# Kernel tuning notes

Measured on AMD Instinct MI355X. Metric: run time of the kernel, lower is better.

Reference implementation:

```python
import jax, jax.numpy as jnp
import numpy as np

N = 50000
E = 800000
DIN = 64
DOUT = 64
H = 4
C = DOUT // H
EPS = 1e-5


def setup_inputs() -> dict:
    key = jax.random.key(0)
    ks = jax.random.split(key, 40)
    inp = {}
    inp["x"] = jax.random.normal(ks[0], (N, DIN), jnp.float32)
    inp["edge_index"] = jax.random.randint(ks[1], (2, E), 0, N, dtype=jnp.int32)
    inp["edge_weight"] = jax.random.uniform(ks[2], (E,), jnp.float32)
    inp["edge_attr"] = jax.random.normal(ks[3], (E, 1), jnp.float32)
    k = 4
    for i in range(2):
        din = DIN if i == 0 else DOUT
        s = din ** -0.5
        inp[f"gcn_w{i}"] = jax.random.normal(ks[k], (din, DOUT), jnp.float32) * s; k += 1
        inp[f"gcn_b{i}"] = jnp.zeros((DOUT,), jnp.float32)
        inp[f"res_w{i}"] = jax.random.normal(ks[k], (din, DOUT), jnp.float32) * s; k += 1
        inp[f"res_b{i}"] = jnp.zeros((DOUT,), jnp.float32)
        inp[f"ln_g{i}"] = jnp.ones((DOUT,), jnp.float32)
        inp[f"ln_b{i}"] = jnp.zeros((DOUT,), jnp.float32)
        sg = DOUT ** -0.5
        inp[f"gat_w{i}"] = jax.random.normal(ks[k], (DOUT, H * C), jnp.float32) * sg; k += 1
        inp[f"gat_b{i}"] = jnp.zeros((H * C,), jnp.float32)
        inp[f"att_src{i}"] = jax.random.normal(ks[k], (H, C), jnp.float32) * (C ** -0.5); k += 1
        inp[f"att_dst{i}"] = jax.random.normal(ks[k], (H, C), jnp.float32) * (C ** -0.5); k += 1
        inp[f"att_e{i}"] = jax.random.normal(ks[k], (H, C), jnp.float32) * (C ** -0.5); k += 1
        inp[f"ew_w{i}"] = jax.random.normal(ks[k], (1, H * C), jnp.float32); k += 1
    return inp


def _gcn(x, src0, dst0, ew, W, b):
    n = x.shape[0]
    sl = jnp.arange(n, dtype=src0.dtype)
    src = jnp.concatenate([src0, sl])
    dst = jnp.concatenate([dst0, sl])
    w = jnp.concatenate([ew, jnp.ones((n,), ew.dtype)])  # self-loop weight 1
    deg = jax.ops.segment_sum(w, dst, num_segments=n)
    dinv = jnp.where(deg > 0, jax.lax.rsqrt(deg), 0.0)
    norm = dinv[src] * w * dinv[dst]
    h = x @ W  # [n, DOUT]
    out = jax.ops.segment_sum(h[src] * norm[:, None], dst, num_segments=n)
    return out + b


def _gat(x, src0, dst0, ea, W, b, a_src, a_dst, a_e, We):
    n = x.shape[0]
    sl = jnp.arange(n, dtype=src0.dtype)
    src = jnp.concatenate([src0, sl])
    dst = jnp.concatenate([dst0, sl])
    loop_attr = jnp.broadcast_to(ea.mean(axis=0, keepdims=True), (n, ea.shape[1]))
    ea2 = jnp.concatenate([ea, loop_attr], axis=0)  # fill_value='mean'
    xl = (x @ W).reshape(n, H, C)
    a_s = (xl * a_src).sum(-1)  # [n,H]
    a_d = (xl * a_dst).sum(-1)
    a_ee = ((ea2 @ We).reshape(-1, H, C) * a_e).sum(-1)  # [E2,H]
    alpha = jax.nn.leaky_relu(a_s[src] + a_d[dst] + a_ee, 0.2)
    m = jax.ops.segment_max(alpha, dst, num_segments=n)
    e = jnp.exp(alpha - m[dst])
    s = jax.ops.segment_sum(e, dst, num_segments=n)
    alpha = e / (s[dst] + 1e-16)
    out = jax.ops.segment_sum(xl[src] * alpha[:, :, None], dst, num_segments=n)
    return out.reshape(n, H * C) + b


def _ln(x, g, b):
    mu = x.mean(-1, keepdims=True)
    v = ((x - mu) ** 2).mean(-1, keepdims=True)
    return (x - mu) * jax.lax.rsqrt(v + EPS) * g + b


def reference(x, edge_index, edge_weight, edge_attr,
              gcn_w0, gcn_b0, res_w0, res_b0, ln_g0, ln_b0,
              gat_w0, gat_b0, att_src0, att_dst0, att_e0, ew_w0,
              gcn_w1, gcn_b1, res_w1, res_b1, ln_g1, ln_b1,
              gat_w1, gat_b1, att_src1, att_dst1, att_e1, ew_w1):
    src0, dst0 = edge_index[0], edge_index[1]
    layers = [
        (gcn_w0, gcn_b0, res_w0, res_b0, ln_g0, ln_b0, gat_w0, gat_b0, att_src0, att_dst0, att_e0, ew_w0),
        (gcn_w1, gcn_b1, res_w1, res_b1, ln_g1, ln_b1, gat_w1, gat_b1, att_src1, att_dst1, att_e1, ew_w1),
    ]
    for (gw, gb, rw, rb, lg, lb, Wg, bg, a_s, a_d, a_e, We) in layers:
        residual = x @ rw + rb
        x = jax.nn.silu(_gcn(x, src0, dst0, edge_weight, gw, gb)) + residual
        x = _ln(x, lg, lb)
        x = jax.nn.silu(_gat(x, src0, dst0, edge_attr, Wg, bg, a_s, a_d, a_e, We)) + x
    return x  # down_sample=False -> Identity
```

## Files before the change

### kernel.cpp

```cpp
#include <hip/hip_runtime.h>
#include <hip/hip_fp16.h>

#define NN 50000
#define NE 800000
#define D 64
#define EPS 1e-5f
#define NT 3125
#define NB1 250
#define EPB 3200
#define NBIN 196
#define STOT 49152
#define SBLK 192

typedef unsigned short ushort_t;
typedef unsigned int uint_t;
typedef __attribute__((ext_vector_type(8))) short bf16x8;
typedef __attribute__((ext_vector_type(4))) float f32x4;

__device__ __forceinline__ float wave_sum64(float v) {
#pragma unroll
  for (int m = 1; m <= 32; m <<= 1) v += __shfl_xor(v, m, 64);
  return v;
}
__device__ __forceinline__ int wave_sum64i(int v) {
#pragma unroll
  for (int m = 1; m <= 32; m <<= 1) v += __shfl_xor(v, m, 64);
  return v;
}
__device__ __forceinline__ float group_sum16(float v) {
#pragma unroll
  for (int m = 1; m <= 8; m <<= 1) v += __shfl_xor(v, m, 64);
  return v;
}
__device__ __forceinline__ float silu_f(float v) { return v / (1.f + __expf(-v)); }
__device__ __forceinline__ float lrelu_f(float v) { return v >= 0.f ? v : 0.2f * v; }
__device__ __forceinline__ ushort_t f2b(float x) {
  unsigned u = __float_as_uint(x);
  return (ushort_t)((u + 0x7FFFu + ((u >> 16) & 1u)) >> 16);
}
__device__ __forceinline__ float b2f(ushort_t u) {
  return __uint_as_float(((unsigned)u) << 16);
}
__device__ __forceinline__ ushort_t f2h(float x) {
  return __half_as_ushort(__float2half_rn(x));
}
__device__ __forceinline__ float h2f(unsigned u) {
  return __half2float(__ushort_as_half((ushort_t)(u & 0xFFFFu)));
}
__device__ __forceinline__ float sel4(float a, float b, float c, float d, int h) {
  float ab = (h & 1) ? b : a;
  float cd = (h & 1) ? d : c;
  return (h & 2) ? cd : ab;
}
__device__ __forceinline__ bf16x8 pack8(float4 a, float4 b) {
  bf16x8 r;
  r[0] = (short)f2b(a.x); r[1] = (short)f2b(a.y);
  r[2] = (short)f2b(a.z); r[3] = (short)f2b(a.w);
  r[4] = (short)f2b(b.x); r[5] = (short)f2b(b.y);
  r[6] = (short)f2b(b.z); r[7] = (short)f2b(b.w);
  return r;
}

__global__ void __launch_bounds__(256) k_pre(
    const int* __restrict__ ei, int* __restrict__ histG,
    const float* __restrict__ x, const float* __restrict__ W1,
    const float* __restrict__ W2, const float* __restrict__ b2,
    ushort_t* __restrict__ out1, float* __restrict__ out2) {
  __shared__ __align__(16) char smem[16384];
  if (blockIdx.x < NB1) {
    int* h = (int*)smem;
    int blk = blockIdx.x;
    for (int j = threadIdx.x; j < NBIN; j += 256) h[j] = 0;
    __syncthreads();
    int e0 = blk * EPB;
    for (int e = e0 + threadIdx.x; e < e0 + EPB; e += 256)
      atomicAdd(&h[ei[NE + e] >> 8], 1);
    __syncthreads();
    for (int j = threadIdx.x; j < NBIN; j += 256) histG[j * NB1 + blk] = h[j];
    return;
  }
  ushort_t* wf = (ushort_t*)smem;
  for (int e = threadIdx.x; e < 8192; e += 256) {
    int f = e >> 9, r = e & 511;
    int lane = r >> 3, j = r & 7;
    int m = f >> 3, s = (f >> 2) & 1, t = f & 3;
    int k = s * 32 + (lane >> 4) * 8 + j;
    int n = t * 16 + (lane & 15);
    const float* Wm = m ? W2 : W1;
    wf[e] = f2b(Wm[k * D + n]);
  }
  __syncthreads();
  int tile = (blockIdx.x - NB1) * 4 + (threadIdx.x >> 6);
  if (tile >= NT) return;
  int l = threadIdx.x & 63;
  int q = l >> 4, cn = l & 15;
  const float* xr = x + ((size_t)tile * 16 + cn) * D + q * 8;
  float4 xa = *(const float4*)xr;
  float4 xb = *(const float4*)(xr + 4);
  float4 xc = *(const float4*)(xr + 32);
  float4 xd = *(const float4*)(xr + 36);
  bf16x8 a0 = pack8(xa, xb), a1 = pack8(xc, xd);
  f32x4 acc1[4], acc2[4];
#pragma unroll
  for (int t = 0; t < 4; ++t) {
    bf16x8 b10 = *(const bf16x8*)&wf[(0 * 8 + 0 * 4 + t) * 512 + l * 8];
    bf16x8 b11 = *(const bf16x8*)&wf[(0 * 8 + 1 * 4 + t) * 512 + l * 8];
    bf16x8 b20 = *(const bf16x8*)&wf[(1 * 8 + 0 * 4 + t) * 512 + l * 8];
    bf16x8 b21 = *(const bf16x8*)&wf[(1 * 8 + 1 * 4 + t) * 512 + l * 8];
    f32x4 z = {0.f, 0.f, 0.f, 0.f};
    acc1[t] = __builtin_amdgcn_mfma_f32_16x16x32_bf16(a0, b10, z, 0, 0, 0);
    acc1[t] = __builtin_amdgcn_mfma_f32_16x16x32_bf16(a1, b11, acc1[t], 0, 0, 0);
    acc2[t] = __builtin_amdgcn_mfma_f32_16x16x32_bf16(a0, b20, z, 0, 0, 0);
    acc2[t] = __builtin_amdgcn_mfma_f32_16x16x32_bf16(a1, b21, acc2[t], 0, 0, 0);
  }
#pragma unroll
  for (int t = 0; t < 4; ++t) {
    float bb = b2[t * 16 + cn];
#pragma unroll
    for (int r = 0; r < 4; ++r) {
      size_t row = (size_t)tile * 16 + q * 4 + r;
      out1[row * D + t * 16 + cn] = f2b(acc1[t][r]);
      out2[row * D + t * 16 + cn] = acc2[t][r] + bb;
    }
  }
}

__global__ void __launch_bounds__(256) k_scanA(
    int* __restrict__ histG, int* __restrict__ bsum, float* __restrict__ scal,
    const float* __restrict__ Wg0, const float* __restrict__ Wg1,
    const float* __restrict__ W11, const float* __restrict__ W21,
    const float* __restrict__ We0, const float* __restrict__ ae0,
    const float* __restrict__ We1, const float* __restrict__ ae1,
    ushort_t* __restrict__ wg16, ushort_t* __restrict__ wd16,
    float* __restrict__ wea2) {
  if (blockIdx.x == SBLK) {
    int tid = threadIdx.x;
    for (int t = tid; t < 1024; t += 256) scal[t] = 0.f;
    for (int e = tid; e < 4096; e += 256) {
      int f = e >> 9, r = e & 511;
      int lane = r >> 3, j = r & 7;
      int s = (f >> 2) & 1, t = f & 3;
      int k = s * 32 + (lane >> 4) * 8 + j;
      int n = t * 16 + (lane & 15);
      wg16[e] = f2b(Wg0[k * D + n]);
      wg16[4096 + e] = f2b(Wg1[k * D + n]);
    }
    for (int e = tid; e < 8192; e += 256) {
      int f = e >> 9, r = e & 511;
      int lane = r >> 3, j = r & 7;
      int m = f >> 3, s = (f >> 2) & 1, t = f & 3;
      int k = s * 32 + (lane >> 4) * 8 + j;
      int n = t * 16 + (lane & 15);
      const float* Wm = m ? W21 : W11;
      wd16[e] = f2b(Wm[k * D + n]);
    }
    if (tid < 64) {
      float v = group_sum16(We0[tid] * ae0[tid]);
      if ((tid & 15) == 0) wea2[tid >> 4] = v;
    } else if (tid < 128) {
      int c = tid - 64;
      float v = group_sum16(We1[c] * ae1[c]);
      if ((c & 15) == 0) wea2[4 + (c >> 4)] = v;
    }
    return;
  }
  __shared__ int sm[256];
  int j = threadIdx.x;
  int i = blockIdx.x * 256 + j;
  const int TOT = NBIN * NB1;
  int v = (i < TOT) ? histG[i] : 0;
  sm[j] = v;
  __syncthreads();
  for (int off = 1; off < 256; off <<= 1) {
    int t = (j >= off) ? sm[j - off] : 0;
    __syncthreads();
    sm[j] += t;
    __syncthreads();
  }
  if (i < TOT) histG[i] = sm[j] - v;
  if (j == 255) bsum[blockIdx.x] = sm[255];
}

__global__ void __launch_bounds__(256) k_scanC(int* __restrict__ histG,
                                               const int* __restrict__ bsum) {
  __shared__ int ws4[4];
  int t = threadIdx.x;
  int v = (t < (int)blockIdx.x) ? bsum[t] : 0;
  v = wave_sum64i(v);
  if ((t & 63) == 0) ws4[t >> 6] = v;
  __syncthreads();
  int prefix = ws4[0] + ws4[1] + ws4[2] + ws4[3];
  int i = blockIdx.x * 256 + t;
  if (i < NBIN * NB1) histG[i] += prefix;
}

__global__ void __launch_bounds__(256) k_part(
    const int* __restrict__ ei, const float* __restrict__ ew,
    const float* __restrict__ ea, const int* __restrict__ histG,
    uint2* __restrict__ rectmp, float* __restrict__ scal) {
  __shared__ int cur[NBIN];
  int blk = blockIdx.x;
  for (int j = threadIdx.x; j < NBIN; j += 256) cur[j] = histG[j * NB1 + blk];
  __syncthreads();
  int e0 = blk * EPB;
  float asum = 0.f;
  for (int e = e0 + threadIdx.x; e < e0 + EPB; e += 256) {
    int src = ei[e];
    int dst = ei[NE + e];
    float w = ew[e];
    float a = ea[e];
    asum += a;
    int slot = atomicAdd(&cur[dst >> 8], 1);
    uint2 r;
    r.x = (uint_t)(src & 0xFFFF) | ((uint_t)f2h(w) << 16);
    r.y = (uint_t)(dst & 0xFF) | ((uint_t)f2h(a) << 16);
    rectmp[slot] = r;
  }
  float s = wave_sum64(asum);
  if ((threadIdx.x & 63) == 0) {
    int slot = (blk * 4 + (threadIdx.x >> 6)) & 63;
    atomicAdd(&scal[(size_t)slot * 16], s);
  }
}

__global__ void __launch_bounds__(256) k_sfin(
    const uint2* __restrict__ rectmp, const int* __restrict__ histG,
    uint2* __restrict__ rec, int* __restrict__ rs,
    float* __restrict__ dinv, float* __restrict__ scal) {
  __shared__ int cnt[256], sc[256], cur[256];
  __shared__ float wsum[256];
  int b = blockIdx.x;
  int t = threadIdx.x;
  int lo = histG[b * NB1];
  int hi = (b == NBIN - 1) ? NE : histG[(b + 1) * NB1];
  cnt[t] = 0;
  wsum[t] = 0.f;
  __syncthreads();
  for (int e = lo + t; e < hi; e += 256)
    atomicAdd(&cnt[rectmp[e].y & 0xFFu], 1);
  __syncthreads();
  int v = cnt[t];
  sc[t] = v;
  __syncthreads();
  for (int off = 1; off < 256; off <<= 1) {
    int u = (t >= off) ? sc[t - off] : 0;
    __syncthreads();
    sc[t] += u;
    __syncthreads();
  }
  int ex = sc[t] - v;
  int node = b * 256 + t;
  if (node < NN) rs[node] = lo + ex;
  if (b == NBIN - 1 && t == 0) rs[NN] = NE;
  cur[t] = lo + ex;
  __syncthreads();
  for (int e = lo + t; e < hi; e += 256) {
    uint2 r = rectmp[e];
    int dl = (int)(r.y & 0xFFu);
    int slot = atomicAdd(&cur[dl], 1);
    atomicAdd(&wsum[dl], h2f(r.x >> 16));
    uint_t src = r.x & 0xFFFFu;
    uint2 o;
    o.x = r.x;
    o.y = src | (r.y & 0xFFFF0000u);
    rec[slot] = o;
  }
  __syncthreads();
  if (node < NN) dinv[node] = rsqrtf(1.f + wsum[t]);
  if (b == 0 && t == 0) {
    float s = 0.f;
    for (int j = 0; j < 64; ++j) s += scal[(size_t)j * 16];
    scal[1] = s / (float)NE;
  }
}

__global__ void __launch_bounds__(256) k_gcn_gat(
    const ushort_t* __restrict__ h16, const float* __restrict__ res,
    const float* __restrict__ dinv, const int* __restrict__ rs,
    const uint_t* __restrict__ rec,
    const float* __restrict__ gb, const float* __restrict__ lg,
    const float* __restrict__ lb,
    const ushort_t* __restrict__ wg, const float* __restrict__ att_src,
    const float* __restrict__ att_dst,
    float* __restrict__ x2, ushort_t* __restrict__ xl,
    float* __restrict__ a_s, float* __restrict__ a_d) {
  __shared__ int ss[4][64];
  __shared__ float swt[4][64];
  __shared__ __align__(16) ushort_t xt[16][72];
  int w = threadIdx.x >> 6;
  int l = threadIdx.x & 63;
  int base = blockIdx.x * 8;
  int iA = base + 2 * w;
  int iB = iA + 1;
  int half = l >> 5, cp = l & 31;
  float diA = dinv[iA], diB = dinv[iB];
  float accA = diA * diA * b2f(h16[(size_t)iA * D + l]);
  float accB = diB * diB * b2f(h16[(size_t)iB * D + l]);
  int kA = rs[iA], kA1 = rs[iA + 1];
  int kB = rs[iB], kB1 = rs[iB + 1];
  while (kA < kA1 || kB < kB1) {
    int cntA = min(32, kA1 - kA);
    int cntB = min(32, kB1 - kB);
    int src = 0; float wn = 0.f;
    if (half == 0) {
      if (cp < cntA) {
        uint_t r = rec[2 * (size_t)(kA + cp)];
        src = (int)(r & 0xFFFFu);
        wn = dinv[src] * h2f(r >> 16) * diA;
      }
    } else {
      if (cp < cntB) {
        uint_t r = rec[2 * (size_t)(kB + cp)];
        src = (int)(r & 0xFFFFu);
        wn = dinv[src] * h2f(r >> 16) * diB;
      }
    }
    ss[w][l] = src;
    swt[w][l] = wn;
    int nm = max(cntA, cntB);
    int j = 0;
    for (; j + 4 <= nm; j += 4) {
      int4 sa = *(const int4*)&ss[w][j];
      int4 sb = *(const int4*)&ss[w][32 + j];
      float4 wa = *(const float4*)&swt[w][j];
      float4 wb = *(const float4*)&swt[w][32 + j];
      float a0 = b2f(h16[(size_t)sa.x * D + l]);
      float b0 = b2f(h16[(size_t)sb.x * D + l]);
      float a1 = b2f(h16[(size_t)sa.y * D + l]);
      float b1 = b2f(h16[(size_t)sb.y * D + l]);
      float a2 = b2f(h16[(size_t)sa.z * D + l]);
      float b2v = b2f(h16[(size_t)sb.z * D + l]);
      float a3 = b2f(h16[(size_t)sa.w * D + l]);
      float b3 = b2f(h16[(size_t)sb.w * D + l]);
      accA = fmaf(wa.x, a0, accA); accB = fmaf(wb.x, b0, accB);
      accA = fmaf(wa.y, a1, accA); accB = fmaf(wb.y, b1, accB);
      accA = fmaf(wa.z, a2, accA); accB = fmaf(wb.z, b2v, accB);
      accA = fmaf(wa.w, a3, accA); accB = fmaf(wb.w, b3, accB);
    }
    for (; j < nm; ++j) {
      int sA = ss[w][j], sB = ss[w][32 + j];
      float wA = swt[w][j], wB = swt[w][32 + j];
      float vA = b2f(h16[(size_t)sA * D + l]);
      float vB = b2f(h16[(size_t)sB * D + l]);
      accA = fmaf(wA, vA, accA);
      accB = fmaf(wB, vB, accB);
    }
    kA += cntA; kB += cntB;
  }
  float gbv = gb[l], lgv = lg[l], lbv = lb[l];
  float x1A = silu_f(accA + gbv) + res[(size_t)iA * D + l];
  float x1B = silu_f(accB + gbv) + res[(size_t)iB * D + l];
  float muA = wave_sum64(x1A) * (1.f / 64.f);
  float muB = wave_sum64(x1B) * (1.f / 64.f);
  float dA = x1A - muA, dB = x1B - muB;
  float varA = wave_sum64(dA * dA) * (1.f / 64.f);
  float varB = wave_sum64(dB * dB) * (1.f / 64.f);
  float oA = dA * rsqrtf(varA + EPS) * lgv + lbv;
  float oB = dB * rsqrtf(varB + EPS) * lgv + lbv;
  x2[(size_t)iA * D + l] = oA;
  x2[(size_t)iB * D + l] = oB;
  xt[2 * w][l] = f2b(oA);
  xt[2 * w + 1][l] = f2b(oB);
  {
    ushort_t* xz = &xt[8][0];
    for (int e = threadIdx.x; e < 8 * 72; e += 256) xz[e] = 0;
  }
  __syncthreads();
  int t = w;
  int q = l >> 4, cn = l & 15;
  bf16x8 a0 = *(const bf16x8*)&xt[cn][q * 8];
  bf16x8 a1 = *(const bf16x8*)&xt[cn][q * 8 + 32];
  bf16x8 b0 = *(const bf16x8*)&wg[(size_t)((0 * 4 + t) * 512 + l * 8)];
  bf16x8 b1 = *(const bf16x8*)&wg[(size_t)((1 * 4 + t) * 512 + l * 8)];
  f32x4 z = {0.f, 0.f, 0.f, 0.f};
  f32x4 acc = __builtin_amdgcn_mfma_f32_16x16x32_bf16(a0, b0, z, 0, 0, 0);
  acc = __builtin_amdgcn_mfma_f32_16x16x32_bf16(a1, b1, acc, 0, 0, 0);
  if (q < 2) {
    float av = att_src[t * 16 + cn];
    float dv = att_dst[t * 16 + cn];
#pragma unroll
    for (int r = 0; r < 4; ++r) {
      size_t row = (size_t)base + q * 4 + r;
      xl[row * D + t * 16 + cn] = f2b(acc[r]);
      float vs = group_sum16(acc[r] * av);
      float vd = group_sum16(acc[r] * dv);
      if (cn == 0) {
        a_s[row * 4 + t] = vs;
        a_d[row * 4 + t] = vd;
      }
    }
  }
}

template <int FUSE>
__global__ void __launch_bounds__(256) k_gat_fin(
    const ushort_t* __restrict__ xl16, const float* __restrict__ x2,
    const float* __restrict__ a_s, const float* __restrict__ a_d,
    const int* __restrict__ rs, const uint_t* __restrict__ rec,
    const float* __restrict__ wea, const float* __restrict__ scal,
    const float* __restrict__ bg,
    const ushort_t* __restrict__ wd, const float* __restrict__ b2,
    ushort_t* __restrict__ out1, float* __restrict__ out2,
    float* __restrict__ xout) {
  __shared__ int ss[4][64];
  __shared__ float el[4][4][68];
  __shared__ __align__(16) ushort_t xt[16][72];
  int w = threadIdx.x >> 6;
  int base = blockIdx.x * 8;
  int iA = base + 2 * w;
  int iB = iA + 1;
  int l = threadIdx.x & 63;
  int half = l >> 5, cp = l & 31;
  int hh = l >> 4;
  float4 wv4 = *(const float4*)wea;
  float mean_attr = scal[1];
  float we_h = sel4(wv4.x, wv4.y, wv4.z, wv4.w, hh);
  float ad_hA = a_d[(size_t)iA * 4 + hh], as_iA = a_s[(size_t)iA * 4 + hh];
  float ad_hB = a_d[(size_t)iB * 4 + hh], as_iB = a_s[(size_t)iB * 4 + hh];
  float eSA = __expf(lrelu_f(as_iA + ad_hA + mean_attr * we_h));
  float eSB = __expf(lrelu_f(as_iB + ad_hB + mean_attr * we_h));
  float sA = eSA, sB = eSB;
  float accA = eSA * b2f(xl16[(size_t)iA * D + l]);
  float accB = eSB * b2f(xl16[(size_t)iB * D + l]);
  const float* adp = a_d + (size_t)(half ? iB : iA) * 4;
  float4 ad4 = *(const float4*)adp;
  int kA = rs[iA], kA1 = rs[iA + 1];
  int kB = rs[iB], kB1 = rs[iB + 1];
  while (kA < kA1 || kB < kB1) {
    int cntA = min(32, kA1 - kA);
    int cntB = min(32, kB1 - kB);
    int myk = half ? kB : kA;
    int mycnt = half ? cntB : cntA;
    int src = 0;
    float e0v = 0.f, e1v = 0.f, e2v = 0.f, e3v = 0.f;
    if (cp < mycnt) {
      uint_t r = rec[2 * (size_t)(myk + cp) + 1];
      src = (int)(r & 0xFFFFu);
      float ea = h2f(r >> 16);
      float4 as4 = *(const float4*)(a_s + (size_t)src * 4);
      e0v = __expf(lrelu_f(as4.x + fmaf(ea, wv4.x, ad4.x)));
      e1v = __expf(lrelu_f(as4.y + fmaf(ea, wv4.y, ad4.y)));
      e2v = __expf(lrelu_f(as4.z + fmaf(ea, wv4.z, ad4.z)));
      e3v = __expf(lrelu_f(as4.w + fmaf(ea, wv4.w, ad4.w)));
    }
    ss[w][l] = src;
    el[w][0][l] = e0v;
    el[w][1][l] = e1v;
    el[w][2][l] = e2v;
    el[w][3][l] = e3v;
    int nm = max(cntA, cntB);
    int j = 0;
    for (; j + 4 <= nm; j += 4) {
      int4 sa = *(const int4*)&ss[w][j];
      int4 sb = *(const int4*)&ss[w][32 + j];
      float4 ea4 = *(const float4*)&el[w][hh][j];
      float4 eb4 = *(const float4*)&el[w][hh][32 + j];
      float a0 = b2f(xl16[(size_t)sa.x * D + l]);
      float b0 = b2f(xl16[(size_t)sb.x * D + l]);
      float a1 = b2f(xl16[(size_t)sa.y * D + l]);
      float b1 = b2f(xl16[(size_t)sb.y * D + l]);
      float a2 = b2f(xl16[(size_t)sa.z * D + l]);
      float b2v = b2f(xl16[(size_t)sb.z * D + l]);
      float a3 = b2f(xl16[(size_t)sa.w * D + l]);
      float b3 = b2f(xl16[(size_t)sb.w * D + l]);
      accA = fmaf(ea4.x, a0, accA); accB = fmaf(eb4.x, b0, accB);
      accA = fmaf(ea4.y, a1, accA); accB = fmaf(eb4.y, b1, accB);
      accA = fmaf(ea4.z, a2, accA); accB = fmaf(eb4.z, b2v, accB);
      accA = fmaf(ea4.w, a3, accA); accB = fmaf(eb4.w, b3, accB);
      sA += (ea4.x + ea4.y) + (ea4.z + ea4.w);
      sB += (eb4.x + eb4.y) + (eb4.z + eb4.w);
    }
    for (; j < nm; ++j) {
      int srcA = ss[w][j], srcB = ss[w][32 + j];
      float eA = el[w][hh][j], eB = el[w][hh][32 + j];
      float vA = b2f(xl16[(size_t)srcA * D + l]);
      float vB = b2f(xl16[(size_t)srcB * D + l]);
      accA = fmaf(eA, vA, accA);
      accB = fmaf(eB, vB, accB);
      sA += eA; sB += eB;
    }
    kA += cntA; kB += cntB;
  }
  float bgv = bg[l];
  float oA = accA / (sA + 1e-16f) + bgv;
  float oB = accB / (sB + 1e-16f) + bgv;
  float vA = silu_f(oA) + x2[(size_t)iA * D + l];
  float vB = silu_f(oB) + x2[(size_t)iB * D + l];
  if (FUSE) {
    xt[2 * w][l] = f2b(vA);
    xt[2 * w + 1][l] = f2b(vB);
    {
      ushort_t* xz = &xt[8][0];
      for (int e = threadIdx.x; e < 8 * 72; e += 256) xz[e] = 0;
    }
    __syncthreads();
    int t = w;
    int q = l >> 4, cn = l & 15;
    bf16x8 a0 = *(const bf16x8*)&xt[cn][q * 8];
    bf16x8 a1 = *(const bf16x8*)&xt[cn][q * 8 + 32];
#pragma unroll
    for (int m = 0; m < 2; ++m) {
      bf16x8 b0 = *(const bf16x8*)&wd[(size_t)((m * 8 + 0 * 4 + t) * 512 + l * 8)];
      bf16x8 b1 = *(const bf16x8*)&wd[(size_t)((m * 8 + 1 * 4 + t) * 512 + l * 8)];
      f32x4 z = {0.f, 0.f, 0.f, 0.f};
      f32x4 acc = __builtin_amdgcn_mfma_f32_16x16x32_bf16(a0, b0, z, 0, 0, 0);
      acc = __builtin_amdgcn_mfma_f32_16x16x32_bf16(a1, b1, acc, 0, 0, 0);
      if (q < 2) {
        float bb = (m == 1) ? b2[t * 16 + cn] : 0.f;
#pragma unroll
        for (int r = 0; r < 4; ++r) {
          size_t row = (size_t)base + q * 4 + r;
          if (m == 0)
            out1[row * D + t * 16 + cn] = f2b(acc[r]);
          else
            out2[row * D + t * 16 + cn] = acc[r] + bb;
        }
      }
    }
  } else {
    xout[(size_t)iA * D + l] = vA;
    xout[(size_t)iB * D + l] = vB;
  }
}


extern "C" void kernel_launch(void* const* d_in, const int* in_sizes, int n_in,
                              void* d_out, int out_size, void* d_ws, size_t ws_size,
                              hipStream_t stream) {
  (void)in_sizes; (void)n_in; (void)out_size; (void)ws_size;
  const float* x  = (const float*)d_in[0];
  const int*   ei = (const int*)d_in[1];
  const float* ew = (const float*)d_in[2];
  const float* ea = (const float*)d_in[3];
  const float* P[2][12];
  for (int l = 0; l < 2; ++l)
    for (int j = 0; j < 12; ++j) P[l][j] = (const float*)d_in[4 + l * 12 + j];

  float* W = (float*)d_ws;
  const size_t o_rs    = 0;
  const size_t o_dinv  = o_rs + NN + 16;
  const size_t o_wea   = o_dinv + NN;
  const size_t o_scal  = o_wea + 16;
  const size_t o_bsum  = o_scal + 1024;
  const size_t o_hist  = o_bsum + 256;
  const size_t o_rec   = o_hist + STOT;
  const size_t o_rtmp  = o_rec + (size_t)NE * 2;
  const size_t o_h16   = o_rtmp + (size_t)NE * 2;
  const size_t o_xl16  = o_h16 + (size_t)NN * D / 2;
  const size_t o_res   = o_xl16 + (size_t)NN * D / 2;
  const size_t o_x2    = o_res + (size_t)NN * D;
  const size_t o_as    = o_x2 + (size_t)NN * D;
  const size_t o_ad    = o_as + (size_t)NN * 4;
  const size_t o_wg16  = o_ad + (size_t)NN * 4;
  const size_t o_wd16  = o_wg16 + 4096;

  int*      rs    = (int*)(W + o_rs);
  float*    dinv  = W + o_dinv;
  float*    wea2  = W + o_wea;
  float*    scal  = W + o_scal;
  int*      bsum  = (int*)(W + o_bsum);
  int*      histG = (int*)(W + o_hist);
  uint2*    rec   = (uint2*)(W + o_rec);
  uint2*    rtmp  = (uint2*)(W + o_rtmp);
  ushort_t* h16   = (ushort_t*)(W + o_h16);
  ushort_t* xl16  = (ushort_t*)(W + o_xl16);
  float*    resb  = W + o_res;
  float*    x2b   = W + o_x2;
  float*    asb   = W + o_as;
  float*    adb   = W + o_ad;
  ushort_t* wg16  = (ushort_t*)(W + o_wg16);
  ushort_t* wd16  = (ushort_t*)(W + o_wd16);

  const int B = 256;
  const int gPre = NB1 + (NT + 3) / 4;
  const int gN2  = NN / 8;

  k_pre<<<gPre, B, 0, stream>>>(ei, histG, x, P[0][0], P[0][2], P[0][3], h16, resb);
  k_scanA<<<SBLK + 1, B, 0, stream>>>(histG, bsum, scal,
                                      P[0][6], P[1][6], P[1][0], P[1][2],
                                      P[0][11], P[0][10], P[1][11], P[1][10],
                                      wg16, wd16, wea2);
  k_scanC<<<SBLK, B, 0, stream>>>(histG, bsum);
  k_part<<<NB1, B, 0, stream>>>(ei, ew, ea, histG, rtmp, scal);
  k_sfin<<<NBIN, B, 0, stream>>>(rtmp, histG, rec, rs, dinv, scal);

  k_gcn_gat<<<gN2, B, 0, stream>>>(h16, resb, dinv, rs, (const uint_t*)rec,
                                   P[0][1], P[0][4], P[0][5],
                                   wg16, P[0][8], P[0][9],
                                   x2b, xl16, asb, adb);
  k_gat_fin<1><<<gN2, B, 0, stream>>>(xl16, x2b, asb, adb, rs, (const uint_t*)rec,
                                      wea2, scal, P[0][7],
                                      wd16, P[1][3], h16, resb, nullptr);
  k_gcn_gat<<<gN2, B, 0, stream>>>(h16, resb, dinv, rs, (const uint_t*)rec,
                                   P[1][1], P[1][4], P[1][5],
                                   wg16 + 4096, P[1][8], P[1][9],
                                   x2b, xl16, asb, adb);
  k_gat_fin<0><<<gN2, B, 0, stream>>>(xl16, x2b, asb, adb, rs, (const uint_t*)rec,
                                      wea2 + 4, scal, P[1][7],
                                      nullptr, nullptr, nullptr, nullptr,
                                      (float*)d_out);
}
```

Measured before the change: 297.0 us.

## Precompute GCN edge norms in CSR build and split edge record arrays

Degree sums move to a global float array filled by atomics in the partition kernel. The CSR finalize kernel then computes each edge's full GCN normalization (dinv[src]*w*dinv[dst]) once, in fp32, and stores it with the source index in a separate 8-byte record array. A separate 4-byte array holds src plus attention edge attribute for the GAT kernels. This removes the per-edge dinv[src] gather and multiply from both GCN aggregation passes and halves the bytes GAT reads per edge. In exchange it adds 800k global float atomics, a per-node zeroing loop run by a single block, and extra random dinv-style reads during the CSR build.

After: 355.0 us. 19.5% more time.

```diff
diff --git a/kernel.cpp b/kernel.cpp
--- a/kernel.cpp
+++ b/kernel.cpp
@@ -132,10 +132,11 @@
     const float* __restrict__ We0, const float* __restrict__ ae0,
     const float* __restrict__ We1, const float* __restrict__ ae1,
     ushort_t* __restrict__ wg16, ushort_t* __restrict__ wd16,
-    float* __restrict__ wea2) {
+    float* __restrict__ wea2, float* __restrict__ degsum) {
   if (blockIdx.x == SBLK) {
     int tid = threadIdx.x;
     for (int t = tid; t < 1024; t += 256) scal[t] = 0.f;
+    for (int t = tid; t < NN; t += 256) degsum[t] = 0.f;
     for (int e = tid; e < 4096; e += 256) {
       int f = e >> 9, r = e & 511;
       int lane = r >> 3, j = r & 7;
@@ -197,7 +198,8 @@
 __global__ void __launch_bounds__(256) k_part(
     const int* __restrict__ ei, const float* __restrict__ ew,
     const float* __restrict__ ea, const int* __restrict__ histG,
-    uint2* __restrict__ rectmp, float* __restrict__ scal) {
+    uint2* __restrict__ rectmp, float* __restrict__ scal,
+    float* __restrict__ degsum) {
   __shared__ int cur[NBIN];
   int blk = blockIdx.x;
   for (int j = threadIdx.x; j < NBIN; j += 256) cur[j] = histG[j * NB1 + blk];
@@ -210,6 +212,7 @@
     float w = ew[e];
     float a = ea[e];
     asum += a;
+    atomicAdd(&degsum[dst], w);
     int slot = atomicAdd(&cur[dst >> 8], 1);
     uint2 r;
     r.x = (uint_t)(src & 0xFFFF) | ((uint_t)f2h(w) << 16);
@@ -225,16 +228,16 @@
 
 __global__ void __launch_bounds__(256) k_sfin(
     const uint2* __restrict__ rectmp, const int* __restrict__ histG,
-    uint2* __restrict__ rec, int* __restrict__ rs,
-    float* __restrict__ dinv, float* __restrict__ scal) {
+    uint2* __restrict__ recw, uint_t* __restrict__ reca, int* __restrict__ rs,
+    float* __restrict__ dinv, const float* __restrict__ degsum,
+    float* __restrict__ scal) {
   __shared__ int cnt[256], sc[256], cur[256];
-  __shared__ float wsum[256];
+  __shared__ float dinvl[256];
   int b = blockIdx.x;
   int t = threadIdx.x;
   int lo = histG[b * NB1];
   int hi = (b == NBIN - 1) ? NE : histG[(b + 1) * NB1];
   cnt[t] = 0;
-  wsum[t] = 0.f;
   __syncthreads();
   for (int e = lo + t; e < hi; e += 256)
     atomicAdd(&cnt[rectmp[e].y & 0xFFu], 1);
@@ -250,7 +253,12 @@
   }
   int ex = sc[t] - v;
   int node = b * 256 + t;
-  if (node < NN) rs[node] = lo + ex;
+  float dloc = (node < NN) ? rsqrtf(1.f + degsum[node]) : 0.f;
+  dinvl[t] = dloc;
+  if (node < NN) {
+    rs[node] = lo + ex;
+    dinv[node] = dloc;
+  }
   if (b == NBIN - 1 && t == 0) rs[NN] = NE;
   cur[t] = lo + ex;
   __syncthreads();
@@ -258,15 +266,15 @@
     uint2 r = rectmp[e];
     int dl = (int)(r.y & 0xFFu);
     int slot = atomicAdd(&cur[dl], 1);
-    atomicAdd(&wsum[dl], h2f(r.x >> 16));
     uint_t src = r.x & 0xFFFFu;
+    float w = h2f(r.x >> 16);
+    float norm = rsqrtf(1.f + degsum[src]) * w * dinvl[dl];
     uint2 o;
-    o.x = r.x;
-    o.y = src | (r.y & 0xFFFF0000u);
-    rec[slot] = o;
-  }
-  __syncthreads();
-  if (node < NN) dinv[node] = rsqrtf(1.f + wsum[t]);
+    o.x = src;
+    o.y = __float_as_uint(norm);
+    recw[slot] = o;
+    reca[slot] = src | (r.y & 0xFFFF0000u);
+  }
   if (b == 0 && t == 0) {
     float s = 0.f;
     for (int j = 0; j < 64; ++j) s += scal[(size_t)j * 16];
@@ -277,7 +285,7 @@
 __global__ void __launch_bounds__(256) k_gcn_gat(
     const ushort_t* __restrict__ h16, const float* __restrict__ res,
     const float* __restrict__ dinv, const int* __restrict__ rs,
-    const uint_t* __restrict__ rec,
+    const uint2* __restrict__ recw,
     const float* __restrict__ gb, const float* __restrict__ lg,
     const float* __restrict__ lb,
     const ushort_t* __restrict__ wg, const float* __restrict__ att_src,
@@ -304,15 +312,15 @@
     int src = 0; float wn = 0.f;
     if (half == 0) {
       if (cp < cntA) {
-        uint_t r = rec[2 * (size_t)(kA + cp)];
-        src = (int)(r & 0xFFFFu);
-        wn = dinv[src] * h2f(r >> 16) * diA;
+        uint2 r = recw[(size_t)(kA + cp)];
+        src = (int)r.x;
+        wn = __uint_as_float(r.y);
       }
     } else {
       if (cp < cntB) {
-        uint_t r = rec[2 * (size_t)(kB + cp)];
-        src = (int)(r & 0xFFFFu);
-        wn = dinv[src] * h2f(r >> 16) * diB;
+        uint2 r = recw[(size_t)(kB + cp)];
+        src = (int)r.x;
+        wn = __uint_as_float(r.y);
       }
     }
     ss[w][l] = src;
@@ -396,7 +404,7 @@
 __global__ void __launch_bounds__(256) k_gat_fin(
     const ushort_t* __restrict__ xl16, const float* __restrict__ x2,
     const float* __restrict__ a_s, const float* __restrict__ a_d,
-    const int* __restrict__ rs, const uint_t* __restrict__ rec,
+    const int* __restrict__ rs, const uint_t* __restrict__ reca,
     const float* __restrict__ wea, const float* __restrict__ scal,
     const float* __restrict__ bg,
     const ushort_t* __restrict__ wd, const float* __restrict__ b2,
@@ -434,7 +442,7 @@
     int src = 0;
     float e0v = 0.f, e1v = 0.f, e2v = 0.f, e3v = 0.f;
     if (cp < mycnt) {
-      uint_t r = rec[2 * (size_t)(myk + cp) + 1];
+      uint_t r = reca[(size_t)(myk + cp)];
       src = (int)(r & 0xFFFFu);
       float ea = h2f(r >> 16);
       float4 as4 = *(const float4*)(a_s + (size_t)src * 4);
@@ -539,12 +547,14 @@
   float* W = (float*)d_ws;
   const size_t o_rs    = 0;
   const size_t o_dinv  = o_rs + NN + 16;
-  const size_t o_wea   = o_dinv + NN;
+  const size_t o_degs  = o_dinv + NN;
+  const size_t o_wea   = o_degs + NN;
   const size_t o_scal  = o_wea + 16;
   const size_t o_bsum  = o_scal + 1024;
   const size_t o_hist  = o_bsum + 256;
-  const size_t o_rec   = o_hist + STOT;
-  const size_t o_rtmp  = o_rec + (size_t)NE * 2;
+  const size_t o_recw  = o_hist + STOT;
+  const size_t o_reca  = o_recw + (size_t)NE * 2;
+  const size_t o_rtmp  = o_reca + NE;
   const size_t o_h16   = o_rtmp + (size_t)NE * 2;
   const size_t o_xl16  = o_h16 + (size_t)NN * D / 2;
   const size_t o_res   = o_xl16 + (size_t)NN * D / 2;
@@ -556,11 +566,13 @@
 
   int*      rs    = (int*)(W + o_rs);
   float*    dinv  = W + o_dinv;
+  float*    degs  = W + o_degs;
   float*    wea2  = W + o_wea;
   float*    scal  = W + o_scal;
   int*      bsum  = (int*)(W + o_bsum);
   int*      histG = (int*)(W + o_hist);
-  uint2*    rec   = (uint2*)(W + o_rec);
+  uint2*    recw  = (uint2*)(W + o_recw);
+  uint_t*   reca  = (uint_t*)(W + o_reca);
   uint2*    rtmp  = (uint2*)(W + o_rtmp);
   ushort_t* h16   = (ushort_t*)(W + o_h16);
   ushort_t* xl16  = (ushort_t*)(W + o_xl16);
@@ -579,23 +591,23 @@
   k_scanA<<<SBLK + 1, B, 0, stream>>>(histG, bsum, scal,
                                       P[0][6], P[1][6], P[1][0], P[1][2],
                                       P[0][11], P[0][10], P[1][11], P[1][10],
-                                      wg16, wd16, wea2);
+                                      wg16, wd16, wea2, degs);
   k_scanC<<<SBLK, B, 0, stream>>>(histG, bsum);
-  k_part<<<NB1, B, 0, stream>>>(ei, ew, ea, histG, rtmp, scal);
-  k_sfin<<<NBIN, B, 0, stream>>>(rtmp, histG, rec, rs, dinv, scal);
-
-  k_gcn_gat<<<gN2, B, 0, stream>>>(h16, resb, dinv, rs, (const uint_t*)rec,
+  k_part<<<NB1, B, 0, stream>>>(ei, ew, ea, histG, rtmp, scal, degs);
+  k_sfin<<<NBIN, B, 0, stream>>>(rtmp, histG, recw, reca, rs, dinv, degs, scal);
+
+  k_gcn_gat<<<gN2, B, 0, stream>>>(h16, resb, dinv, rs, recw,
                                    P[0][1], P[0][4], P[0][5],
                                    wg16, P[0][8], P[0][9],
                                    x2b, xl16, asb, adb);
-  k_gat_fin<1><<<gN2, B, 0, stream>>>(xl16, x2b, asb, adb, rs, (const uint_t*)rec,
+  k_gat_fin<1><<<gN2, B, 0, stream>>>(xl16, x2b, asb, adb, rs, reca,
                                       wea2, scal, P[0][7],
                                       wd16, P[1][3], h16, resb, nullptr);
-  k_gcn_gat<<<gN2, B, 0, stream>>>(h16, resb, dinv, rs, (const uint_t*)rec,
+  k_gcn_gat<<<gN2, B, 0, stream>>>(h16, resb, dinv, rs, recw,
                                    P[1][1], P[1][4], P[1][5],
                                    wg16 + 4096, P[1][8], P[1][9],
                                    x2b, xl16, asb, adb);
-  k_gat_fin<0><<<gN2, B, 0, stream>>>(xl16, x2b, asb, adb, rs, (const uint_t*)rec,
+  k_gat_fin<0><<<gN2, B, 0, stream>>>(xl16, x2b, asb, adb, rs, reca,
                                       wea2 + 4, scal, P[1][7],
                                       nullptr, nullptr, nullptr, nullptr,
                                       (float*)d_out);
```
